# Kernel optimization log

Hardware: AMD Instinct MI355X
Metric: run time of the kernel (lower is better)

## Reference

```python
import jax, jax.numpy as jnp
import numpy as np

B, N, C_IN = 8, 8192, 64
M, K, RADIUS = 1024, 64, 0.2
MLP = [64, 64, 128]


def _fps(pts, m):
    """Iterative farthest point sampling. pts: [N,3] -> [m] int32 indices."""
    n = pts.shape[0]

    def step(carry, _):
        dists, last = carry
        d = jnp.sum((pts - pts[last]) ** 2, axis=-1)          # [N]
        dists = jnp.minimum(dists, d)
        nxt = jnp.argmax(dists).astype(jnp.int32)
        return (dists, nxt), nxt

    init = (jnp.full((n,), 1e10, pts.dtype), jnp.int32(0))
    _, idx = jax.lax.scan(step, init, None, length=m - 1)
    return jnp.concatenate([jnp.zeros((1,), jnp.int32), idx])


def _ball_query(new_xyz, xyz, radius, k):
    """new_xyz: [B,3,M], xyz: [B,3,N] -> [B,M,K] neighbor indices.
    First k points within radius (in index order); padded with first hit."""
    d2 = (jnp.sum(new_xyz ** 2, 1)[:, :, None] + jnp.sum(xyz ** 2, 1)[:, None, :]
          - 2.0 * jnp.einsum('bcm,bcn->bmn', new_xyz, xyz))   # [B,M,N]
    mask = d2 < radius * radius
    # stable argsort of ~mask puts indices of in-radius points first, in order
    order = jnp.argsort(jnp.where(mask, 0, 1).astype(jnp.int32), axis=-1)[..., :k]
    count = jnp.sum(mask, axis=-1)                             # [B,M]
    valid = jnp.arange(k)[None, None, :] < count[..., None]
    return jnp.where(valid, order, order[..., :1])


def _group(x, idx):
    """x: [B,C,N], idx: [B,...] -> [B,C,...] gathered along N."""
    return jax.vmap(lambda a, i: a[:, i])(x, idx)


def _forward(xyz, feature, params):
    # FPS centroid indices (torch runs under no_grad -> stop_gradient)
    pts = jax.lax.stop_gradient(jnp.transpose(xyz, (0, 2, 1)))  # [B,N,3]
    cidx = jax.vmap(lambda p: _fps(p, M))(pts)                  # [B,M]
    new_xyz = _group(xyz, cidx)                                 # [B,3,M]
    nidx = _ball_query(jax.lax.stop_gradient(new_xyz),
                       jax.lax.stop_gradient(xyz), RADIUS, K)   # [B,M,K]
    gxyz = _group(xyz, nidx) - new_xyz[..., None]               # [B,3,M,K]
    x = jnp.concatenate([gxyz, _group(feature, nidx)], axis=1)  # [B,3+C,M,K]
    # SharedMLP: 1x1 conv2d + BN (folded to per-channel scale/bias) + ReLU
    for w, s, b in params:
        x = jax.nn.relu(jnp.einsum('oi,bimk->bomk', w, x)
                        * s[:, None, None] + b[:, None, None])
    return new_xyz, jnp.max(x, axis=3)                          # [B,3,M], [B,128,M]


def setup_inputs() -> dict:
    key = jax.random.key(0)
    ks = jax.random.split(key, 5)
    inp = {
        'xyz': jax.random.normal(ks[0], (B, 3, N), jnp.float32),
        'feature': jax.random.normal(ks[1], (B, C_IN, N), jnp.float32),
    }
    prev = C_IN + 3  # use_xyz=True
    for li, co in enumerate(MLP):
        inp[f'w{li}'] = jax.random.normal(ks[2 + li], (co, prev), jnp.float32) / np.sqrt(prev).astype(np.float32)
        inp[f's{li}'] = jnp.ones((co,), jnp.float32)
        inp[f'b{li}'] = jnp.zeros((co,), jnp.float32)
        prev = co
    return inp


def reference(xyz, feature, w0, s0, b0, w1, s1, b1, w2, s2, b2):
    return _forward(xyz, feature, ((w0, s0, b0), (w1, s1, b1), (w2, s2, b2)))
```

## Files before the change

kernel.cpp:

```cpp
#include <hip/hip_runtime.h>


#define B_ 8
#define N_ 8192
#define M_ 1024
#define K_ 64
#define FTW 68

typedef float vf2 __attribute__((ext_vector_type(2)));

template <int CTRL>
__device__ __forceinline__ unsigned long long dpp_key(unsigned long long k) {
  int lo = __builtin_amdgcn_update_dpp(0, (int)(unsigned int)k, CTRL, 0xF, 0xF, true);
  int hi = __builtin_amdgcn_update_dpp(0, (int)(unsigned int)(k >> 32), CTRL, 0xF, 0xF, true);
  unsigned long long o = ((unsigned long long)(unsigned int)hi << 32) | (unsigned int)lo;
  return o > k ? o : k;
}

__global__ __launch_bounds__(256) void fps_ft_kernel(const float* __restrict__ xyz,
                                                     const float* __restrict__ feat,
                                                     float* __restrict__ ft,
                                                     float* __restrict__ nxyz) {
#pragma clang fp contract(off)
  if (blockIdx.x >= 8) {
    const int nb = gridDim.x - 8;
    const int total = B_ * N_ * FTW;
    for (int idx = (blockIdx.x - 8) * 256 + threadIdx.x; idx < total; idx += nb * 256) {
      int c = idx % FTW;
      int bn = idx / FTW;
      int n = bn & (N_ - 1);
      int b = bn >> 13;
      float v;
      if (c < 3) v = xyz[(b * 3 + c) * N_ + n];
      else if (c < 67) v = feat[(b * 64 + (c - 3)) * N_ + n];
      else v = 0.f;
      ft[idx] = v;
    }
    return;
  }

  __shared__ float4 pts4[N_];
  __shared__ unsigned long long cand[2][16];
  __shared__ int scidx[M_];
  const int b = blockIdx.x;
  const int t = threadIdx.x;
  const int lane = t & 63;
  const int wid = t >> 6;
  const float* xb = xyz + b * 3 * N_;

  for (int n = t; n < N_; n += 256) {
    pts4[n] = make_float4(xb[n], xb[N_ + n], xb[2 * N_ + n], 0.f);
  }

  const int base = t * 32;
  const vf2* xv = (const vf2*)(xb + base);
  const vf2* yv = (const vf2*)(xb + N_ + base);
  const vf2* zv = (const vf2*)(xb + 2 * N_ + base);
  vf2 px2[16], py2[16], pz2[16], mind2[16];
#pragma unroll
  for (int j = 0; j < 16; ++j) {
    px2[j] = xv[j];
    py2[j] = yv[j];
    pz2[j] = zv[j];
    mind2[j] = vf2{1e10f, 1e10f};
  }
  float xl = xb[0], yl = xb[N_], zl = xb[2 * N_];
  if (t == 0) scidx[0] = 0;
  __syncthreads();

  for (int i = 1; i < M_; ++i) {
    const vf2 xl2 = vf2{xl, xl}, yl2 = vf2{yl, yl}, zl2 = vf2{zl, zl};
    float bestv = -1.f;
    int bl = 0;
#pragma unroll
    for (int j = 0; j < 16; ++j) {
      vf2 dx = px2[j] - xl2;
      vf2 dy = py2[j] - yl2;
      vf2 dz = pz2[j] - zl2;
      vf2 d = (dx * dx + dy * dy) + dz * dz;
      vf2 md;
      md.x = fminf(mind2[j].x, d.x);
      md.y = fminf(mind2[j].y, d.y);
      mind2[j] = md;
      if (md.x > bestv) { bestv = md.x; bl = 2 * j; }
      if (md.y > bestv) { bestv = md.y; bl = 2 * j + 1; }
    }
    unsigned long long key =
        ((unsigned long long)__float_as_uint(bestv) << 32) | (unsigned int)(~(base + bl));
    key = dpp_key<0xB1>(key);
    key = dpp_key<0x4E>(key);
    key = dpp_key<0x141>(key);
    key = dpp_key<0x140>(key);
    if ((lane & 15) == 0) cand[i & 1][wid * 4 + (lane >> 4)] = key;
    __syncthreads();
    unsigned long long gk = cand[i & 1][lane & 15];
    gk = dpp_key<0xB1>(gk);
    gk = dpp_key<0x4E>(gk);
    gk = dpp_key<0x141>(gk);
    gk = dpp_key<0x140>(gk);
    const int gi = (int)(~(unsigned int)gk);
    if (t == 0) scidx[i] = gi;
    float4 cc = pts4[gi];
    xl = cc.x; yl = cc.y; zl = cc.z;
  }
  __syncthreads();
  for (int q = t; q < M_; q += 256) {
    int ci = scidx[q];
    float4 c = pts4[ci];
    nxyz[b * 3 * M_ + q] = c.x;
    nxyz[b * 3 * M_ + M_ + q] = c.y;
    nxyz[b * 3 * M_ + 2 * M_ + q] = c.z;
  }
}

__global__ __launch_bounds__(256) void ballq_kernel(const float* __restrict__ xyz,
                                                    const float* __restrict__ nxyz,
                                                    int* __restrict__ nidx) {
  const int lane = threadIdx.x & 63;
  const int g = blockIdx.x * 4 + (threadIdx.x >> 6);
  const int b = g >> 10;
  const int m = g & (M_ - 1);
  const float* xb = xyz + b * 3 * N_;
  const float cx = nxyz[b * 3 * M_ + m];
  const float cy = nxyz[b * 3 * M_ + M_ + m];
  const float cz = nxyz[b * 3 * M_ + 2 * M_ + m];
  const float nc = __fadd_rn(__fadd_rn(__fmul_rn(cx, cx), __fmul_rn(cy, cy)), __fmul_rn(cz, cz));
  int cnt = 0;
  int first = 0;
  int* slot = nidx + (g << 6);
  for (int basei = 0; basei < N_ && cnt < K_; basei += 64) {
    const int n = basei + lane;
    float p_x = xb[n], p_y = xb[N_ + n], p_z = xb[2 * N_ + n];
    float pn = __fadd_rn(__fadd_rn(__fmul_rn(p_x, p_x), __fmul_rn(p_y, p_y)), __fmul_rn(p_z, p_z));
    float dt = __fadd_rn(__fadd_rn(__fmul_rn(cx, p_x), __fmul_rn(cy, p_y)), __fmul_rn(cz, p_z));
    float d2 = __fsub_rn(__fadd_rn(nc, pn), __fmul_rn(2.f, dt));
    bool inr = d2 < 0.04f;
    unsigned long long mk = __ballot(inr);
    if (cnt == 0 && mk != 0ull) first = basei + (__ffsll((long long)mk) - 1);
    int pos = cnt + (int)__popcll(mk & ((1ull << lane) - 1ull));
    if (inr && pos < K_) slot[pos] = n;
    cnt += (int)__popcll(mk);
  }
  if (cnt > K_) cnt = K_;
  if (lane >= cnt) slot[lane] = first;
}

template <bool USE_FT>
__global__ __launch_bounds__(64) void mlp_kernel(
    const float* __restrict__ ft, const float* __restrict__ xyz, const float* __restrict__ feat,
    const int* __restrict__ nidx, const float* __restrict__ nxyz,
    const float* __restrict__ w0, const float* __restrict__ s0, const float* __restrict__ b0,
    const float* __restrict__ w1, const float* __restrict__ s1, const float* __restrict__ b1,
    const float* __restrict__ w2, const float* __restrict__ s2, const float* __restrict__ b2,
    float* __restrict__ out2) {
  __shared__ float ylds[64 * 65];
  const int g = blockIdx.x;
  const int b = g >> 10;
  const int m = g & (M_ - 1);
  const int lane = threadIdx.x;
  const int n = nidx[(g << 6) + lane];
  const float cx = nxyz[b * 3 * M_ + m];
  const float cy = nxyz[b * 3 * M_ + M_ + m];
  const float cz = nxyz[b * 3 * M_ + 2 * M_ + m];

  float x0[67];
  if (USE_FT) {
    const float4* row = (const float4*)(ft + (size_t)((b << 13) + n) * FTW);
    float f[FTW];
#pragma unroll
    for (int q = 0; q < 17; ++q) {
      float4 v = row[q];
      f[q * 4 + 0] = v.x; f[q * 4 + 1] = v.y; f[q * 4 + 2] = v.z; f[q * 4 + 3] = v.w;
    }
    x0[0] = f[0] - cx; x0[1] = f[1] - cy; x0[2] = f[2] - cz;
#pragma unroll
    for (int c = 3; c < 67; ++c) x0[c] = f[c];
  } else {
    const float* xb = xyz + b * 3 * N_;
    x0[0] = xb[n] - cx; x0[1] = xb[N_ + n] - cy; x0[2] = xb[2 * N_ + n] - cz;
#pragma unroll
    for (int c = 0; c < 64; ++c) x0[3 + c] = feat[((b << 6) + c) * N_ + n];
  }

  for (int o = 0; o < 64; o += 4) {
    const float* wr = w0 + o * 67;
    float a0 = 0.f, a1 = 0.f, a2 = 0.f, a3 = 0.f;
#pragma unroll
    for (int ci = 0; ci < 67; ++ci) {
      float xvv = x0[ci];
      a0 = fmaf(wr[ci], xvv, a0);
      a1 = fmaf(wr[67 + ci], xvv, a1);
      a2 = fmaf(wr[134 + ci], xvv, a2);
      a3 = fmaf(wr[201 + ci], xvv, a3);
    }
    ylds[lane * 65 + o + 0] = fmaxf(fmaf(a0, s0[o + 0], b0[o + 0]), 0.f);
    ylds[lane * 65 + o + 1] = fmaxf(fmaf(a1, s0[o + 1], b0[o + 1]), 0.f);
    ylds[lane * 65 + o + 2] = fmaxf(fmaf(a2, s0[o + 2], b0[o + 2]), 0.f);
    ylds[lane * 65 + o + 3] = fmaxf(fmaf(a3, s0[o + 3], b0[o + 3]), 0.f);
  }
  float x1[64];
#pragma unroll
  for (int c = 0; c < 64; ++c) x1[c] = ylds[lane * 65 + c];

  for (int o = 0; o < 64; o += 4) {
    const float* wr = w1 + o * 64;
    float a0 = 0.f, a1 = 0.f, a2 = 0.f, a3 = 0.f;
#pragma unroll
    for (int ci = 0; ci < 64; ++ci) {
      float xvv = x1[ci];
      a0 = fmaf(wr[ci], xvv, a0);
      a1 = fmaf(wr[64 + ci], xvv, a1);
      a2 = fmaf(wr[128 + ci], xvv, a2);
      a3 = fmaf(wr[192 + ci], xvv, a3);
    }
    ylds[lane * 65 + o + 0] = fmaxf(fmaf(a0, s1[o + 0], b1[o + 0]), 0.f);
    ylds[lane * 65 + o + 1] = fmaxf(fmaf(a1, s1[o + 1], b1[o + 1]), 0.f);
    ylds[lane * 65 + o + 2] = fmaxf(fmaf(a2, s1[o + 2], b1[o + 2]), 0.f);
    ylds[lane * 65 + o + 3] = fmaxf(fmaf(a3, s1[o + 3], b1[o + 3]), 0.f);
  }
  float x2[64];
#pragma unroll
  for (int c = 0; c < 64; ++c) x2[c] = ylds[lane * 65 + c];

  float* outbm = out2 + (size_t)(b * 128) * M_ + m;
  for (int o = 0; o < 128; o += 4) {
    const float* wr = w2 + o * 64;
    float a0 = 0.f, a1 = 0.f, a2 = 0.f, a3 = 0.f;
#pragma unroll
    for (int ci = 0; ci < 64; ++ci) {
      float xvv = x2[ci];
      a0 = fmaf(wr[ci], xvv, a0);
      a1 = fmaf(wr[64 + ci], xvv, a1);
      a2 = fmaf(wr[128 + ci], xvv, a2);
      a3 = fmaf(wr[192 + ci], xvv, a3);
    }
    float v0 = fmaxf(fmaf(a0, s2[o + 0], b2[o + 0]), 0.f);
    float v1 = fmaxf(fmaf(a1, s2[o + 1], b2[o + 1]), 0.f);
    float v2 = fmaxf(fmaf(a2, s2[o + 2], b2[o + 2]), 0.f);
    float v3 = fmaxf(fmaf(a3, s2[o + 3], b2[o + 3]), 0.f);
#pragma unroll
    for (int off = 32; off > 0; off >>= 1) {
      v0 = fmaxf(v0, __shfl_xor(v0, off, 64));
      v1 = fmaxf(v1, __shfl_xor(v1, off, 64));
      v2 = fmaxf(v2, __shfl_xor(v2, off, 64));
      v3 = fmaxf(v3, __shfl_xor(v3, off, 64));
    }
    if (lane == ((o + 0) & 63)) outbm[(o + 0) * M_] = v0;
    if (lane == ((o + 1) & 63)) outbm[(o + 1) * M_] = v1;
    if (lane == ((o + 2) & 63)) outbm[(o + 2) * M_] = v2;
    if (lane == ((o + 3) & 63)) outbm[(o + 3) * M_] = v3;
  }
}

extern "C" void kernel_launch(void* const* d_in, const int* in_sizes, int n_in,
                              void* d_out, int out_size, void* d_ws, size_t ws_size,
                              hipStream_t stream) {
  const float* xyz = (const float*)d_in[0];
  const float* feat = (const float*)d_in[1];
  const float* w0 = (const float*)d_in[2];
  const float* s0 = (const float*)d_in[3];
  const float* b0 = (const float*)d_in[4];
  const float* w1 = (const float*)d_in[5];
  const float* s1 = (const float*)d_in[6];
  const float* b1 = (const float*)d_in[7];
  const float* w2 = (const float*)d_in[8];
  const float* s2 = (const float*)d_in[9];
  const float* b2 = (const float*)d_in[10];

  float* nxyz = (float*)d_out;
  float* out2 = (float*)d_out + B_ * 3 * M_;

  const size_t nidx_bytes = (size_t)B_ * M_ * K_ * sizeof(int);
  const size_t ft_bytes = (size_t)B_ * N_ * FTW * sizeof(float);
  int* nidx = (int*)d_ws;
  float* ft = (float*)((char*)d_ws + nidx_bytes);
  const bool use_ft = ws_size >= nidx_bytes + ft_bytes;

  hipLaunchKernelGGL(fps_ft_kernel, dim3(use_ft ? 64 : 8), dim3(256), 0, stream,
                     xyz, feat, ft, nxyz);
  hipLaunchKernelGGL(ballq_kernel, dim3(B_ * M_ / 4), dim3(256), 0, stream, xyz, nxyz, nidx);
  if (use_ft) {
    hipLaunchKernelGGL((mlp_kernel<true>), dim3(B_ * M_), dim3(64), 0, stream,
                       ft, xyz, feat, nidx, nxyz, w0, s0, b0, w1, s1, b1, w2, s2, b2, out2);
  } else {
    hipLaunchKernelGGL((mlp_kernel<false>), dim3(B_ * M_), dim3(64), 0, stream,
                       ft, xyz, feat, nidx, nxyz, w0, s0, b0, w1, s1, b1, w2, s2, b2, out2);
  }
}
```

Baseline: 1.398 ms.

## Use packed f32 asm in FPS, full-wave DPP reductions, register-only MLP layers

The FPS distance update is forced onto v_pk_add/v_pk_mul packed FP32 instructions. The per-wave argmax now reduces across all 64 lanes with DPP row_bcast, so the cross-wave stage only needs 4 candidates and two DPP steps. In the MLP kernel, the first two layers are fully unrolled in registers with no LDS staging, and the final max-over-neighbours uses DPP plus readlane instead of shuffles. The fully unrolled register layers risk high VGPR pressure or spills, and the inline asm limits how the compiler can schedule the FPS loop.

```diff
diff --git a/kernel.cpp b/kernel.cpp
--- a/kernel.cpp
+++ b/kernel.cpp
@@ -8,6 +8,17 @@
 #define FTW 68
 
 typedef float vf2 __attribute__((ext_vector_type(2)));
+
+__device__ __forceinline__ vf2 pk_add(vf2 a, vf2 b) {
+  vf2 d;
+  asm("v_pk_add_f32 %0, %1, %2" : "=v"(d) : "v"(a), "v"(b));
+  return d;
+}
+__device__ __forceinline__ vf2 pk_mul(vf2 a, vf2 b) {
+  vf2 d;
+  asm("v_pk_mul_f32 %0, %1, %2" : "=v"(d) : "v"(a), "v"(b));
+  return d;
+}
 
 template <int CTRL>
 __device__ __forceinline__ unsigned long long dpp_key(unsigned long long k) {
@@ -15,6 +26,21 @@
   int hi = __builtin_amdgcn_update_dpp(0, (int)(unsigned int)(k >> 32), CTRL, 0xF, 0xF, true);
   unsigned long long o = ((unsigned long long)(unsigned int)hi << 32) | (unsigned int)lo;
   return o > k ? o : k;
+}
+
+template <int CTRL>
+__device__ __forceinline__ float dpp_fmax(float v) {
+  int o = __builtin_amdgcn_update_dpp(0, __float_as_int(v), CTRL, 0xF, 0xF, true);
+  return fmaxf(v, __int_as_float(o));
+}
+__device__ __forceinline__ float wave_fmax63(float v) {
+  v = dpp_fmax<0xB1>(v);
+  v = dpp_fmax<0x4E>(v);
+  v = dpp_fmax<0x141>(v);
+  v = dpp_fmax<0x140>(v);
+  v = dpp_fmax<0x142>(v);
+  v = dpp_fmax<0x143>(v);
+  return v;
 }
 
 __global__ __launch_bounds__(256) void fps_ft_kernel(const float* __restrict__ xyz,
@@ -40,7 +66,7 @@
   }
 
   __shared__ float4 pts4[N_];
-  __shared__ unsigned long long cand[2][16];
+  __shared__ unsigned long long cand[2][4];
   __shared__ int scidx[M_];
   const int b = blockIdx.x;
   const int t = threadIdx.x;
@@ -69,15 +95,16 @@
   __syncthreads();
 
   for (int i = 1; i < M_; ++i) {
-    const vf2 xl2 = vf2{xl, xl}, yl2 = vf2{yl, yl}, zl2 = vf2{zl, zl};
+    const float nx = -xl, ny = -yl, nz = -zl;
+    const vf2 nx2 = vf2{nx, nx}, ny2 = vf2{ny, ny}, nz2 = vf2{nz, nz};
     float bestv = -1.f;
     int bl = 0;
 #pragma unroll
     for (int j = 0; j < 16; ++j) {
-      vf2 dx = px2[j] - xl2;
-      vf2 dy = py2[j] - yl2;
-      vf2 dz = pz2[j] - zl2;
-      vf2 d = (dx * dx + dy * dy) + dz * dz;
+      vf2 dx = pk_add(px2[j], nx2);
+      vf2 dy = pk_add(py2[j], ny2);
+      vf2 dz = pk_add(pz2[j], nz2);
+      vf2 d = pk_add(pk_add(pk_mul(dx, dx), pk_mul(dy, dy)), pk_mul(dz, dz));
       vf2 md;
       md.x = fminf(mind2[j].x, d.x);
       md.y = fminf(mind2[j].y, d.y);
@@ -91,13 +118,13 @@
     key = dpp_key<0x4E>(key);
     key = dpp_key<0x141>(key);
     key = dpp_key<0x140>(key);
-    if ((lane & 15) == 0) cand[i & 1][wid * 4 + (lane >> 4)] = key;
+    key = dpp_key<0x142>(key);
+    key = dpp_key<0x143>(key);
+    if (lane == 63) cand[i & 1][wid] = key;
     __syncthreads();
-    unsigned long long gk = cand[i & 1][lane & 15];
+    unsigned long long gk = cand[i & 1][lane & 3];
     gk = dpp_key<0xB1>(gk);
     gk = dpp_key<0x4E>(gk);
-    gk = dpp_key<0x141>(gk);
-    gk = dpp_key<0x140>(gk);
     const int gi = (int)(~(unsigned int)gk);
     if (t == 0) scidx[i] = gi;
     float4 cc = pts4[gi];
@@ -153,7 +180,6 @@
     const float* __restrict__ w1, const float* __restrict__ s1, const float* __restrict__ b1,
     const float* __restrict__ w2, const float* __restrict__ s2, const float* __restrict__ b2,
     float* __restrict__ out2) {
-  __shared__ float ylds[64 * 65];
   const int g = blockIdx.x;
   const int b = g >> 10;
   const int m = g & (M_ - 1);
@@ -182,45 +208,23 @@
     for (int c = 0; c < 64; ++c) x0[3 + c] = feat[((b << 6) + c) * N_ + n];
   }
 
-  for (int o = 0; o < 64; o += 4) {
-    const float* wr = w0 + o * 67;
-    float a0 = 0.f, a1 = 0.f, a2 = 0.f, a3 = 0.f;
-#pragma unroll
-    for (int ci = 0; ci < 67; ++ci) {
-      float xvv = x0[ci];
-      a0 = fmaf(wr[ci], xvv, a0);
-      a1 = fmaf(wr[67 + ci], xvv, a1);
-      a2 = fmaf(wr[134 + ci], xvv, a2);
-      a3 = fmaf(wr[201 + ci], xvv, a3);
-    }
-    ylds[lane * 65 + o + 0] = fmaxf(fmaf(a0, s0[o + 0], b0[o + 0]), 0.f);
-    ylds[lane * 65 + o + 1] = fmaxf(fmaf(a1, s0[o + 1], b0[o + 1]), 0.f);
-    ylds[lane * 65 + o + 2] = fmaxf(fmaf(a2, s0[o + 2], b0[o + 2]), 0.f);
-    ylds[lane * 65 + o + 3] = fmaxf(fmaf(a3, s0[o + 3], b0[o + 3]), 0.f);
-  }
   float x1[64];
 #pragma unroll
-  for (int c = 0; c < 64; ++c) x1[c] = ylds[lane * 65 + c];
-
-  for (int o = 0; o < 64; o += 4) {
-    const float* wr = w1 + o * 64;
-    float a0 = 0.f, a1 = 0.f, a2 = 0.f, a3 = 0.f;
-#pragma unroll
-    for (int ci = 0; ci < 64; ++ci) {
-      float xvv = x1[ci];
-      a0 = fmaf(wr[ci], xvv, a0);
-      a1 = fmaf(wr[64 + ci], xvv, a1);
-      a2 = fmaf(wr[128 + ci], xvv, a2);
-      a3 = fmaf(wr[192 + ci], xvv, a3);
-    }
-    ylds[lane * 65 + o + 0] = fmaxf(fmaf(a0, s1[o + 0], b1[o + 0]), 0.f);
-    ylds[lane * 65 + o + 1] = fmaxf(fmaf(a1, s1[o + 1], b1[o + 1]), 0.f);
-    ylds[lane * 65 + o + 2] = fmaxf(fmaf(a2, s1[o + 2], b1[o + 2]), 0.f);
-    ylds[lane * 65 + o + 3] = fmaxf(fmaf(a3, s1[o + 3], b1[o + 3]), 0.f);
-  }
+  for (int o = 0; o < 64; ++o) {
+    float acc = 0.f;
+#pragma unroll
+    for (int ci = 0; ci < 67; ++ci) acc = fmaf(w0[o * 67 + ci], x0[ci], acc);
+    x1[o] = fmaxf(fmaf(acc, s0[o], b0[o]), 0.f);
+  }
+
   float x2[64];
 #pragma unroll
-  for (int c = 0; c < 64; ++c) x2[c] = ylds[lane * 65 + c];
+  for (int o = 0; o < 64; ++o) {
+    float acc = 0.f;
+#pragma unroll
+    for (int ci = 0; ci < 64; ++ci) acc = fmaf(w1[o * 64 + ci], x1[ci], acc);
+    x2[o] = fmaxf(fmaf(acc, s1[o], b1[o]), 0.f);
+  }
 
   float* outbm = out2 + (size_t)(b * 128) * M_ + m;
   for (int o = 0; o < 128; o += 4) {
@@ -238,17 +242,18 @@
     float v1 = fmaxf(fmaf(a1, s2[o + 1], b2[o + 1]), 0.f);
     float v2 = fmaxf(fmaf(a2, s2[o + 2], b2[o + 2]), 0.f);
     float v3 = fmaxf(fmaf(a3, s2[o + 3], b2[o + 3]), 0.f);
-#pragma unroll
-    for (int off = 32; off > 0; off >>= 1) {
-      v0 = fmaxf(v0, __shfl_xor(v0, off, 64));
-      v1 = fmaxf(v1, __shfl_xor(v1, off, 64));
-      v2 = fmaxf(v2, __shfl_xor(v2, off, 64));
-      v3 = fmaxf(v3, __shfl_xor(v3, off, 64));
-    }
-    if (lane == ((o + 0) & 63)) outbm[(o + 0) * M_] = v0;
-    if (lane == ((o + 1) & 63)) outbm[(o + 1) * M_] = v1;
-    if (lane == ((o + 2) & 63)) outbm[(o + 2) * M_] = v2;
-    if (lane == ((o + 3) & 63)) outbm[(o + 3) * M_] = v3;
+    v0 = wave_fmax63(v0);
+    v1 = wave_fmax63(v1);
+    v2 = wave_fmax63(v2);
+    v3 = wave_fmax63(v3);
+    float g0 = __int_as_float(__builtin_amdgcn_readlane(__float_as_int(v0), 63));
+    float g1 = __int_as_float(__builtin_amdgcn_readlane(__float_as_int(v1), 63));
+    float g2 = __int_as_float(__builtin_amdgcn_readlane(__float_as_int(v2), 63));
+    float g3 = __int_as_float(__builtin_amdgcn_readlane(__float_as_int(v3), 63));
+    if (lane == ((o + 0) & 63)) outbm[(o + 0) * M_] = g0;
+    if (lane == ((o + 1) & 63)) outbm[(o + 1) * M_] = g1;
+    if (lane == ((o + 2) & 63)) outbm[(o + 2) * M_] = g2;
+    if (lane == ((o + 3) & 63)) outbm[(o + 3) * M_] = g3;
   }
 }
 
```

New measurement: 1.540 ms. 10.1% more time.
